# Kernel tuning notes

Hardware: AMD Instinct MI355X
Metric: run time of the kernel (lower is better)

## Reference

```python
import jax, jax.numpy as jnp
import numpy as np

B, L, D, H = 2, 2048, 1024, 16
Dh = D // H


def setup_inputs() -> dict:
    key = jax.random.key(0)
    k = jax.random.split(key, 6)
    s = 1.0 / np.sqrt(D).astype(np.float32)
    return {
        "x": jax.random.normal(k[0], (B, L, D), jnp.float32),
        "mask": jnp.ones((B, L), jnp.int32),
        "user_emb": jax.random.normal(k[1], (B, D), jnp.float32),
        "W_q": jax.random.normal(k[2], (D, D), jnp.float32) * s,
        "W_k": jax.random.normal(k[3], (D, D), jnp.float32) * s,
        "W_v": jax.random.normal(k[4], (D, D), jnp.float32) * s,
        "W_o": jax.random.normal(k[5], (D, D), jnp.float32) * s,
    }


def reference(x, mask, user_emb, W_q, W_k, W_v, W_o):
    b, l, d = x.shape
    # torch nn.Linear(bias=False): y = x @ W.T
    Q = x @ W_q.T
    K = x @ W_k.T
    V = x @ W_v.T

    def split(t):  # [B,L,D] -> [B,H,L,Dh]
        return t.reshape(b, l, H, Dh).transpose(0, 2, 1, 3)

    Qh, Kh, Vh = split(Q), split(K), split(V)

    # additive_bias: rank-1 per-head user bias, [B,H,L,1]
    u = user_emb.reshape(b, H, Dh)
    bias = jnp.einsum('bhld,bhd->bhl', Qh, u)[..., None]

    scores = jnp.einsum('bhld,bhmd->bhlm', Qh, Kh) / np.float32(np.sqrt(Dh))
    scores = scores + bias
    # padding mask: 1 = valid, 0 = pad (broadcast over query dim)
    scores = jnp.where(mask[:, None, None, :] == 0, -jnp.inf, scores)
    # causal mask
    causal = jnp.triu(jnp.ones((l, l), jnp.bool_), k=1)
    scores = jnp.where(causal, -jnp.inf, scores)

    attn = jax.nn.softmax(scores, axis=-1)  # dropout p=0 -> identity
    ctx = jnp.einsum('bhlm,bhmd->bhld', attn, Vh)
    out = ctx.transpose(0, 2, 1, 3).reshape(b, l, d)
    return out @ W_o.T
```

## Files before the change

### kernel.cpp

```cpp
#include <hip/hip_runtime.h>
#include <hip/hip_bf16.h>
#include <stdint.h>

#define Bc 2
#define Lc 2048
#define Dc 1024
#define Hc 16
#define DHc 64

using f32x4  = __attribute__((ext_vector_type(4))) float;
using f32x16 = __attribute__((ext_vector_type(16))) float;
using bf16x8 = __attribute__((ext_vector_type(8))) short;
using bf16x4 = __attribute__((ext_vector_type(4))) short;

static __device__ __forceinline__ unsigned short f2bf(float f) {
  __hip_bfloat16 h = __float2bfloat16(f);
  return __builtin_bit_cast(unsigned short, h);
}
static __device__ __forceinline__ float bf2f(unsigned short u) {
  unsigned int x = ((unsigned int)u) << 16;
  return __builtin_bit_cast(float, x);
}
static __device__ __forceinline__ unsigned int pk2(float a, float b) {
  return (unsigned int)f2bf(a) | ((unsigned int)f2bf(b) << 16);
}

static __device__ __forceinline__ void gload16(const void* g, void* l) {
  __builtin_amdgcn_global_load_lds(
      (const __attribute__((address_space(1))) unsigned int*)g,
      (__attribute__((address_space(3))) unsigned int*)l, 16, 0, 0);
}

__global__ __launch_bounds__(256) void cvt_kernel(
    const float* __restrict__ x,  const float* __restrict__ wq,
    const float* __restrict__ wk, const float* __restrict__ wv,
    const float* __restrict__ wo,
    unsigned short* __restrict__ xb,  unsigned short* __restrict__ wqb,
    unsigned short* __restrict__ wkb, unsigned short* __restrict__ wvb,
    unsigned short* __restrict__ wob) {
  int i = (blockIdx.x * 256 + threadIdx.x) * 4;
  const float* src; unsigned short* dst; int off;
  if (i < 4194304) { src = x; dst = xb; off = i; }
  else {
    int j = i - 4194304; int w = j >> 20; off = j & 1048575;
    src = w == 0 ? wq : w == 1 ? wk : w == 2 ? wv : wo;
    dst = w == 0 ? wqb : w == 1 ? wkb : w == 2 ? wvb : wob;
  }
  float4 v = *(const float4*)(src + off);
  ushort4 u;
  u.x = f2bf(v.x); u.y = f2bf(v.y); u.z = f2bf(v.z); u.w = f2bf(v.w);
  *(ushort4*)(dst + off) = u;
}

template <int MODE>
static __device__ __forceinline__ void gemm_body(
    const unsigned short* __restrict__ A, const unsigned short* __restrict__ Bw,
    void* __restrict__ Cout, float scale, char* As, char* Bs, int tm, int tn) {
  const int t = threadIdx.x, w = t >> 6, l = t & 63;
  const int wr = w >> 1, wc = w & 1;
  const int K = 1024;
  f32x4 zz = {0.f, 0.f, 0.f, 0.f};
  f32x4 acc[4][4];
  for (int a = 0; a < 4; a++)
    for (int b = 0; b < 4; b++) acc[a][b] = zz;
  const char* Ag = (const char*)A;
  const char* Bg = (const char*)Bw;
  for (int k0 = 0; k0 < K; k0 += 32) {
#pragma unroll
    for (int i = 0; i < 2; i++) {
      int s = i * 256 + w * 64 + l;
      gload16(Ag + ((tm + (s >> 2)) * K + k0 + (s & 3) * 8) * 2,
              As + (i * 256 + w * 64) * 16);
      gload16(Bg + ((tn + (s >> 2)) * K + k0 + (s & 3) * 8) * 2,
              Bs + (i * 256 + w * 64) * 16);
    }
    __syncthreads();
    bf16x8 af[4], bfg[4];
#pragma unroll
    for (int mm = 0; mm < 4; mm++)
      af[mm] = *(const bf16x8*)(As + (wr * 64 + mm * 16 + (l & 15)) * 64 + (l >> 4) * 16);
#pragma unroll
    for (int nn = 0; nn < 4; nn++)
      bfg[nn] = *(const bf16x8*)(Bs + (wc * 64 + nn * 16 + (l & 15)) * 64 + (l >> 4) * 16);
#pragma unroll
    for (int mm = 0; mm < 4; mm++)
#pragma unroll
      for (int nn = 0; nn < 4; nn++)
        acc[mm][nn] = __builtin_amdgcn_mfma_f32_16x16x32_bf16(af[mm], bfg[nn], acc[mm][nn], 0, 0, 0);
    __syncthreads();
  }
#pragma unroll
  for (int mm = 0; mm < 4; mm++) {
#pragma unroll
    for (int nn = 0; nn < 4; nn++) {
      int col = tn + wc * 64 + nn * 16 + (l & 15);
#pragma unroll
      for (int r = 0; r < 4; r++) {
        int row = tm + wr * 64 + mm * 16 + (l >> 4) * 4 + r;
        if (MODE == 0) {
          int b = row >> 11, ll = row & 2047, h = col >> 6, d = col & 63;
          ((unsigned short*)Cout)[(((b * Hc + h) << 11) + ll) * 64 + d] =
              f2bf(acc[mm][nn][r] * scale);
        } else if (MODE == 1) {
          ((float*)Cout)[row * 1024 + col] = acc[mm][nn][r];
        } else {
          int h = row >> 6, d = row & 63, b = col >> 11, ll = col & 2047;
          ((unsigned short*)Cout)[(((b * Hc + h) * 64 + d) << 11) + ll] =
              f2bf(acc[mm][nn][r]);
        }
      }
    }
  }
}

__global__ __launch_bounds__(256) void gemm_qkv(
    const unsigned short* __restrict__ xb,
    const unsigned short* __restrict__ wq, const unsigned short* __restrict__ wk,
    const unsigned short* __restrict__ wv,
    unsigned short* __restrict__ q, unsigned short* __restrict__ k,
    unsigned short* __restrict__ vT) {
  __shared__ char lds[16384];
  int z = blockIdx.z;
  if (z < 2) {
    gemm_body<0>(xb, z == 0 ? wq : wk, z == 0 ? q : k,
                 z == 0 ? 0.125f * 1.44269504089f : 1.0f,
                 lds, lds + 8192, blockIdx.x * 128, blockIdx.y * 128);
  } else {
    gemm_body<2>(wv, xb, vT, 1.0f, lds, lds + 8192,
                 blockIdx.y * 128, blockIdx.x * 128);
  }
}

__global__ __launch_bounds__(256) void gemm_out(
    const unsigned short* __restrict__ ctx, const unsigned short* __restrict__ wo,
    float* __restrict__ out) {
  __shared__ char lds[16384];
  gemm_body<1>(ctx, wo, out, 1.0f, lds, lds + 8192,
               blockIdx.x * 128, blockIdx.y * 128);
}

__global__ __launch_bounds__(256, 4) void attn_kernel(
    const unsigned short* __restrict__ Q, const unsigned short* __restrict__ Kg,
    const unsigned short* __restrict__ VT,
    unsigned short* __restrict__ Op, float2* __restrict__ ml) {
  __shared__ char lds[32768];
  const int t = threadIdx.x, w = t >> 6, l = t & 63;
  const int hi = l >> 5, q32 = l & 31;
  const int idx = blockIdx.x;
  const int bh = idx & 31;
  const int g = idx >> 5;
  const int qt = 15 - (g >> 1);
  const int c = g & 1;
  const int h1 = qt + 1;
  const int kb0 = c ? h1 : 0;
  const int kb1 = c ? 2 * h1 : h1;
  const unsigned short* Qb = Q + bh * (Lc * DHc);
  const unsigned short* Kb = Kg + bh * (Lc * DHc);
  const unsigned short* Vb = VT + bh * (Lc * DHc);
  const int qrow = qt * 128 + w * 32 + q32;

  bf16x8 qf[4];
#pragma unroll
  for (int s = 0; s < 4; s++)
    qf[s] = *(const bf16x8*)(Qb + qrow * 64 + s * 16 + hi * 8);

  const f32x16 z16 = {0.f,0.f,0.f,0.f,0.f,0.f,0.f,0.f,
                      0.f,0.f,0.f,0.f,0.f,0.f,0.f,0.f};
  float mi = -1e30f, li = 0.f;
  f32x16 accO[2];
  accO[0] = z16; accO[1] = z16;

  const int s0i = w * 64 + l;
  auto stage = [&](int bi, int kb) {
    char* Ksb = lds + bi * 8192;
    char* Vsb = lds + 16384 + bi * 8192;
#pragma unroll
    for (int i = 0; i < 2; i++) {
      int s = i * 256 + s0i;
      int row = s >> 3;
      int cb = ((s & 7) * 16) ^ ((row & 7) << 4);
      gload16((const char*)Kb + (kb * 64 + row) * 128 + cb,
              Ksb + (i * 256 + w * 64) * 16);
      gload16((const char*)Vb + row * 4096 + kb * 128 + cb,
              Vsb + (i * 256 + w * 64) * 16);
    }
  };

  stage(0, kb0);
  __syncthreads();
  for (int kb = kb0; kb < kb1; ++kb) {
    const int cur = (kb - kb0) & 1;
    char* Ks = lds + cur * 8192;
    char* Vs = lds + 16384 + cur * 8192;
    if (kb + 1 < kb1) stage(cur ^ 1, kb + 1);

    f32x16 sf[2];
    sf[0] = z16; sf[1] = z16;
    __builtin_amdgcn_s_setprio(1);
#pragma unroll
    for (int blk = 0; blk < 2; blk++) {
      int row = blk * 32 + q32;
      int rsw = (row & 7) << 4;
#pragma unroll
      for (int s = 0; s < 4; s++) {
        bf16x8 kf = *(const bf16x8*)(Ks + row * 128 + (((2 * s + hi) * 16) ^ rsw));
        sf[blk] = __builtin_amdgcn_mfma_f32_32x32x16_bf16(kf, qf[s], sf[blk], 0, 0, 0);
      }
    }
    __builtin_amdgcn_s_setprio(0);

    if (kb * 64 + 63 > qt * 128 + w * 32) {
#pragma unroll
      for (int blk = 0; blk < 2; blk++)
#pragma unroll
        for (int r = 0; r < 16; r++) {
          int kg = kb * 64 + blk * 32 + (r & 3) + 8 * (r >> 2) + 4 * hi;
          if (kg > qrow) sf[blk][r] = -1e30f;
        }
    }

    float tm16[16];
#pragma unroll
    for (int r = 0; r < 16; r++) tm16[r] = fmaxf(sf[0][r], sf[1][r]);
#pragma unroll
    for (int r = 0; r < 8; r++) tm16[r] = fmaxf(tm16[r], tm16[r + 8]);
#pragma unroll
    for (int r = 0; r < 4; r++) tm16[r] = fmaxf(tm16[r], tm16[r + 4]);
    float pm = fmaxf(fmaxf(tm16[0], tm16[1]), fmaxf(tm16[2], tm16[3]));
    pm = fmaxf(pm, __shfl_xor(pm, 32));

    if (!__all(pm - mi <= 8.f)) {
      float corr = __builtin_amdgcn_exp2f(mi - pm);
      mi = pm;
      li *= corr;
#pragma unroll
      for (int db = 0; db < 2; db++)
#pragma unroll
        for (int r = 0; r < 16; r++) accO[db][r] *= corr;
    }

    float a16[16];
#pragma unroll
    for (int r = 0; r < 16; r++) {
      float p0 = __builtin_amdgcn_exp2f(sf[0][r] - mi);
      float p1 = __builtin_amdgcn_exp2f(sf[1][r] - mi);
      sf[0][r] = p0; sf[1][r] = p1;
      a16[r] = p0 + p1;
    }
#pragma unroll
    for (int r = 0; r < 8; r++) a16[r] += a16[r + 8];
#pragma unroll
    for (int r = 0; r < 4; r++) a16[r] += a16[r + 4];
    float rs = (a16[0] + a16[1]) + (a16[2] + a16[3]);
    rs += __shfl_xor(rs, 32);
    li += rs;

    bf16x8 pf[4];
#pragma unroll
    for (int kw = 0; kw < 4; kw++) {
      const int bkl = kw >> 1, o = (kw & 1) * 8;
      unsigned int a01 = pk2(sf[bkl][o + 0], sf[bkl][o + 1]);
      unsigned int a23 = pk2(sf[bkl][o + 2], sf[bkl][o + 3]);
      unsigned int b01 = pk2(sf[bkl][o + 4], sf[bkl][o + 5]);
      unsigned int b23 = pk2(sf[bkl][o + 6], sf[bkl][o + 7]);
      auto s1 = __builtin_amdgcn_permlane32_swap(a01, b01, false, false);
      auto s2 = __builtin_amdgcn_permlane32_swap(a23, b23, false, false);
      uint4 uu;
      uu.x = s1[0];
      uu.y = s2[0];
      uu.z = s1[1];
      uu.w = s2[1];
      pf[kw] = __builtin_bit_cast(bf16x8, uu);
    }

    __builtin_amdgcn_s_setprio(1);
#pragma unroll
    for (int kw = 0; kw < 4; kw++) {
#pragma unroll
      for (int db = 0; db < 2; db++) {
        int row = db * 32 + q32;
        int rsw = (row & 7) << 4;
        bf16x8 vf = *(const bf16x8*)(Vs + row * 128 + (((2 * kw + hi) * 16) ^ rsw));
        accO[db] = __builtin_amdgcn_mfma_f32_32x32x16_bf16(vf, pf[kw], accO[db], 0, 0, 0);
      }
    }
    __builtin_amdgcn_s_setprio(0);
    __syncthreads();
  }

  unsigned short* Opc = Op + idx * 8192;
  const int ql = w * 32 + q32;
#pragma unroll
  for (int db = 0; db < 2; db++)
#pragma unroll
    for (int rq = 0; rq < 4; rq++) {
      int d0 = db * 32 + 8 * rq + 4 * hi;
      bf16x4 v4;
#pragma unroll
      for (int j = 0; j < 4; j++) v4[j] = (short)f2bf(accO[db][rq * 4 + j]);
      *(bf16x4*)(Opc + ql * 64 + d0) = v4;
    }
  if (hi == 0) ml[idx * 128 + ql] = make_float2(mi, li);
}

__global__ __launch_bounds__(256) void combine_kernel(
    const unsigned short* __restrict__ Op, const float2* __restrict__ ml,
    unsigned short* __restrict__ ctx) {
  const int cb = blockIdx.x;
  const int bh = cb & 31, qt = cb >> 5;
  const int i0 = ((15 - qt) * 2) * 32 + bh;
  const int i1 = i0 + 32;
  const int t = threadIdx.x;
  const int ql = t >> 1, dh = (t & 1) * 32;
  float2 p0 = ml[i0 * 128 + ql];
  float2 p1 = ml[i1 * 128 + ql];
  float m = fmaxf(p0.x, p1.x);
  float e0 = __builtin_amdgcn_exp2f(p0.x - m);
  float e1 = __builtin_amdgcn_exp2f(p1.x - m);
  float inv = 1.0f / (p0.y * e0 + p1.y * e1);
  float s0 = e0 * inv, s1 = e1 * inv;
  const int b = bh >> 4, h = bh & 15;
  unsigned short* dst = ctx + (size_t)(b * Lc + qt * 128 + ql) * Dc + h * 64 + dh;
  const unsigned short* q0 = Op + i0 * 8192 + ql * 64 + dh;
  const unsigned short* q1 = Op + i1 * 8192 + ql * 64 + dh;
#pragma unroll
  for (int seg = 0; seg < 4; seg++) {
    bf16x8 o0 = *(const bf16x8*)(q0 + seg * 8);
    bf16x8 o1 = *(const bf16x8*)(q1 + seg * 8);
    bf16x8 outv;
#pragma unroll
    for (int j = 0; j < 8; j++)
      outv[j] = (short)f2bf(bf2f((unsigned short)o0[j]) * s0 +
                            bf2f((unsigned short)o1[j]) * s1);
    *(bf16x8*)(dst + seg * 8) = outv;
  }
}

extern "C" void kernel_launch(void* const* d_in, const int* in_sizes, int n_in,
                              void* d_out, int out_size, void* d_ws, size_t ws_size,
                              hipStream_t stream) {
  const float* x  = (const float*)d_in[0];
  const float* Wq = (const float*)d_in[3];
  const float* Wk = (const float*)d_in[4];
  const float* Wv = (const float*)d_in[5];
  const float* Wo = (const float*)d_in[6];

  char* ws = (char*)d_ws;
  const size_t MB = 1024 * 1024;
  unsigned short* xb  = (unsigned short*)(ws);
  unsigned short* wqb = (unsigned short*)(ws + 8 * MB);
  unsigned short* wkb = (unsigned short*)(ws + 10 * MB);
  unsigned short* wvb = (unsigned short*)(ws + 12 * MB);
  unsigned short* q   = (unsigned short*)(ws + 16 * MB);
  unsigned short* k   = (unsigned short*)(ws + 24 * MB);
  unsigned short* vT  = (unsigned short*)(ws + 32 * MB);
  unsigned short* ctx = (unsigned short*)(ws + 40 * MB);
  unsigned short* wob = (unsigned short*)(ws + 48 * MB);
  unsigned short* Op  = (unsigned short*)(ws);
  float2*         ml  = (float2*)(ws + 50 * MB);

  cvt_kernel<<<8192, 256, 0, stream>>>(x, Wq, Wk, Wv, Wo, xb, wqb, wkb, wvb, wob);
  gemm_qkv<<<dim3(32, 8, 3), 256, 0, stream>>>(xb, wqb, wkb, wvb, q, k, vT);
  attn_kernel<<<1024, 256, 0, stream>>>(q, k, vT, Op, ml);
  combine_kernel<<<512, 256, 0, stream>>>(Op, ml, ctx);
  gemm_out<<<dim3(32, 8, 1), 256, 0, stream>>>(ctx, wob, (float*)d_out);
}
```

Measured before the change: 110.1 us.

## Rebalance causal attention split-K work via lookup table and write unsplit tiles directly

Replaces the uniform two-way split of each query tile's key range with a 36-entry table of (query tile, key range) chunks. Short tiles run unsplit and write normalized context directly, while long tiles are split into 2-4 chunks that the combine kernel merges, for 1152 roughly equal-sized blocks. It also swaps one __syncthreads per iteration for explicit vmcnt waits plus s_barrier so the prefetch of the next tile can stay in flight, and uses v_cvt_pk_bf16_f32 for packing. The aim is to cut tail imbalance and combine traffic, at the cost of table lookups and a combine over a variable number of chunks.

```diff
diff --git a/kernel.cpp b/kernel.cpp
--- a/kernel.cpp
+++ b/kernel.cpp
@@ -21,8 +21,10 @@
   unsigned int x = ((unsigned int)u) << 16;
   return __builtin_bit_cast(float, x);
 }
-static __device__ __forceinline__ unsigned int pk2(float a, float b) {
-  return (unsigned int)f2bf(a) | ((unsigned int)f2bf(b) << 16);
+static __device__ __forceinline__ unsigned int cvtpk(float a, float b) {
+  unsigned int r;
+  asm("v_cvt_pk_bf16_f32 %0, %1, %2" : "=v"(r) : "v"(a), "v"(b));
+  return r;
 }
 
 static __device__ __forceinline__ void gload16(const void* g, void* l) {
@@ -139,21 +141,26 @@
                blockIdx.x * 128, blockIdx.y * 128);
 }
 
+__device__ const int g_qt[36]  = {7,6,5,15,15,15,15,14,14,11,11,11,10,4,13,13,13,13,14,14,12,12,10,10,9,9,3,12,12,9,8,8,8,2,1,0};
+__device__ const int g_kb0[36] = {0,0,0,0,8,16,24,0,8,0,8,16,0,0,0,7,14,21,16,23,0,7,8,15,0,7,0,14,20,14,0,6,12,0,0,0};
+__device__ const int g_kb1[36] = {16,14,12,8,16,24,32,8,16,8,16,24,8,10,7,14,21,28,23,30,7,14,15,22,7,14,8,20,26,20,6,12,18,6,4,2};
+__device__ const int g_pid[36] = {-1,-1,-1,0,1,2,3,4,5,16,17,18,19,-1,8,9,10,11,6,7,12,13,20,21,22,23,-1,14,15,24,25,26,27,-1,-1,-1};
+
 __global__ __launch_bounds__(256, 4) void attn_kernel(
     const unsigned short* __restrict__ Q, const unsigned short* __restrict__ Kg,
     const unsigned short* __restrict__ VT,
-    unsigned short* __restrict__ Op, float2* __restrict__ ml) {
+    unsigned short* __restrict__ Op, float2* __restrict__ ml,
+    unsigned short* __restrict__ ctx) {
   __shared__ char lds[32768];
   const int t = threadIdx.x, w = t >> 6, l = t & 63;
   const int hi = l >> 5, q32 = l & 31;
   const int idx = blockIdx.x;
   const int bh = idx & 31;
   const int g = idx >> 5;
-  const int qt = 15 - (g >> 1);
-  const int c = g & 1;
-  const int h1 = qt + 1;
-  const int kb0 = c ? h1 : 0;
-  const int kb1 = c ? 2 * h1 : h1;
+  const int qt  = g_qt[g];
+  const int kb0 = g_kb0[g];
+  const int kb1 = g_kb1[g];
+  const int pid = g_pid[g];
   const unsigned short* Qb = Q + bh * (Lc * DHc);
   const unsigned short* Kb = Kg + bh * (Lc * DHc);
   const unsigned short* Vb = VT + bh * (Lc * DHc);
@@ -187,12 +194,19 @@
   };
 
   stage(0, kb0);
-  __syncthreads();
   for (int kb = kb0; kb < kb1; ++kb) {
     const int cur = (kb - kb0) & 1;
     char* Ks = lds + cur * 8192;
     char* Vs = lds + 16384 + cur * 8192;
-    if (kb + 1 < kb1) stage(cur ^ 1, kb + 1);
+    if (kb + 1 < kb1) {
+      stage(cur ^ 1, kb + 1);
+      asm volatile("s_waitcnt vmcnt(4)" ::: "memory");
+    } else {
+      asm volatile("s_waitcnt vmcnt(0)" ::: "memory");
+    }
+    __builtin_amdgcn_sched_barrier(0);
+    __builtin_amdgcn_s_barrier();
+    __builtin_amdgcn_sched_barrier(0);
 
     f32x16 sf[2];
     sf[0] = z16; sf[1] = z16;
@@ -259,10 +273,10 @@
 #pragma unroll
     for (int kw = 0; kw < 4; kw++) {
       const int bkl = kw >> 1, o = (kw & 1) * 8;
-      unsigned int a01 = pk2(sf[bkl][o + 0], sf[bkl][o + 1]);
-      unsigned int a23 = pk2(sf[bkl][o + 2], sf[bkl][o + 3]);
-      unsigned int b01 = pk2(sf[bkl][o + 4], sf[bkl][o + 5]);
-      unsigned int b23 = pk2(sf[bkl][o + 6], sf[bkl][o + 7]);
+      unsigned int a01 = cvtpk(sf[bkl][o + 0], sf[bkl][o + 1]);
+      unsigned int a23 = cvtpk(sf[bkl][o + 2], sf[bkl][o + 3]);
+      unsigned int b01 = cvtpk(sf[bkl][o + 4], sf[bkl][o + 5]);
+      unsigned int b23 = cvtpk(sf[bkl][o + 6], sf[bkl][o + 7]);
       auto s1 = __builtin_amdgcn_permlane32_swap(a01, b01, false, false);
       auto s2 = __builtin_amdgcn_permlane32_swap(a23, b23, false, false);
       uint4 uu;
@@ -285,53 +299,89 @@
       }
     }
     __builtin_amdgcn_s_setprio(0);
-    __syncthreads();
-  }
-
-  unsigned short* Opc = Op + idx * 8192;
-  const int ql = w * 32 + q32;
-#pragma unroll
-  for (int db = 0; db < 2; db++)
-#pragma unroll
-    for (int rq = 0; rq < 4; rq++) {
-      int d0 = db * 32 + 8 * rq + 4 * hi;
-      bf16x4 v4;
-#pragma unroll
-      for (int j = 0; j < 4; j++) v4[j] = (short)f2bf(accO[db][rq * 4 + j]);
-      *(bf16x4*)(Opc + ql * 64 + d0) = v4;
-    }
-  if (hi == 0) ml[idx * 128 + ql] = make_float2(mi, li);
-}
+    __builtin_amdgcn_sched_barrier(0);
+    __builtin_amdgcn_s_barrier();
+  }
+
+  const int b = bh >> 4, h = bh & 15;
+  if (pid < 0) {
+    float inv = 1.0f / li;
+    unsigned short* dst = ctx + (size_t)(b * Lc + qrow) * Dc + h * 64;
+#pragma unroll
+    for (int db = 0; db < 2; db++)
+#pragma unroll
+      for (int rq = 0; rq < 4; rq++) {
+        int d0 = db * 32 + 8 * rq + 4 * hi;
+        bf16x4 v4;
+#pragma unroll
+        for (int j = 0; j < 4; j++) v4[j] = (short)f2bf(accO[db][rq * 4 + j] * inv);
+        *(bf16x4*)(dst + d0) = v4;
+      }
+  } else {
+    unsigned short* Opc = Op + (size_t)(bh * 28 + pid) * 8192;
+    const int ql = w * 32 + q32;
+#pragma unroll
+    for (int db = 0; db < 2; db++)
+#pragma unroll
+      for (int rq = 0; rq < 4; rq++) {
+        int d0 = db * 32 + 8 * rq + 4 * hi;
+        bf16x4 v4;
+#pragma unroll
+        for (int j = 0; j < 4; j++) v4[j] = (short)f2bf(accO[db][rq * 4 + j]);
+        *(bf16x4*)(Opc + ql * 64 + d0) = v4;
+      }
+    if (hi == 0) ml[(bh * 28 + pid) * 128 + ql] = make_float2(mi, li);
+  }
+}
+
+__device__ const int c_pb[8]  = {25, 22, 19, 16, 12, 8, 4, 0};
+__device__ const int c_nch[8] = { 3,  3,  3,  3,  4, 4, 4, 4};
 
 __global__ __launch_bounds__(256) void combine_kernel(
     const unsigned short* __restrict__ Op, const float2* __restrict__ ml,
     unsigned short* __restrict__ ctx) {
   const int cb = blockIdx.x;
-  const int bh = cb & 31, qt = cb >> 5;
-  const int i0 = ((15 - qt) * 2) * 32 + bh;
-  const int i1 = i0 + 32;
+  const int qq = cb >> 5, bh = cb & 31;
+  const int qt = 8 + qq;
+  const int pb = c_pb[qq], nch = c_nch[qq];
   const int t = threadIdx.x;
   const int ql = t >> 1, dh = (t & 1) * 32;
-  float2 p0 = ml[i0 * 128 + ql];
-  float2 p1 = ml[i1 * 128 + ql];
-  float m = fmaxf(p0.x, p1.x);
-  float e0 = __builtin_amdgcn_exp2f(p0.x - m);
-  float e1 = __builtin_amdgcn_exp2f(p1.x - m);
-  float inv = 1.0f / (p0.y * e0 + p1.y * e1);
-  float s0 = e0 * inv, s1 = e1 * inv;
+  float2 pp[4];
+  float mx = -1e30f;
+#pragma unroll
+  for (int j = 0; j < 4; j++) {
+    int jj = j < nch ? j : 0;
+    float2 v = ml[(size_t)(bh * 28 + pb + jj) * 128 + ql];
+    pp[j] = (j < nch) ? v : make_float2(-1e30f, 0.f);
+    mx = fmaxf(mx, pp[j].x);
+  }
+  float wgt[4];
+  float den = 0.f;
+#pragma unroll
+  for (int j = 0; j < 4; j++) {
+    float e = __builtin_amdgcn_exp2f(pp[j].x - mx);
+    den += pp[j].y * e;
+    wgt[j] = e;
+  }
+  float inv = 1.0f / den;
+#pragma unroll
+  for (int j = 0; j < 4; j++) wgt[j] *= inv;
   const int b = bh >> 4, h = bh & 15;
   unsigned short* dst = ctx + (size_t)(b * Lc + qt * 128 + ql) * Dc + h * 64 + dh;
-  const unsigned short* q0 = Op + i0 * 8192 + ql * 64 + dh;
-  const unsigned short* q1 = Op + i1 * 8192 + ql * 64 + dh;
 #pragma unroll
   for (int seg = 0; seg < 4; seg++) {
-    bf16x8 o0 = *(const bf16x8*)(q0 + seg * 8);
-    bf16x8 o1 = *(const bf16x8*)(q1 + seg * 8);
+    float a8[8] = {0.f, 0.f, 0.f, 0.f, 0.f, 0.f, 0.f, 0.f};
+#pragma unroll
+    for (int j = 0; j < 4; j++) {
+      int jj = j < nch ? j : 0;
+      bf16x8 o = *(const bf16x8*)(Op + (size_t)(bh * 28 + pb + jj) * 8192 +
+                                  ql * 64 + dh + seg * 8);
+#pragma unroll
+      for (int e = 0; e < 8; e++) a8[e] += wgt[j] * bf2f((unsigned short)o[e]);
+    }
     bf16x8 outv;
 #pragma unroll
-    for (int j = 0; j < 8; j++)
-      outv[j] = (short)f2bf(bf2f((unsigned short)o0[j]) * s0 +
-                            bf2f((unsigned short)o1[j]) * s1);
+    for (int e = 0; e < 8; e++) outv[e] = (short)f2bf(a8[e]);
     *(bf16x8*)(dst + seg * 8) = outv;
   }
 }
@@ -361,7 +411,7 @@
 
   cvt_kernel<<<8192, 256, 0, stream>>>(x, Wq, Wk, Wv, Wo, xb, wqb, wkb, wvb, wob);
   gemm_qkv<<<dim3(32, 8, 3), 256, 0, stream>>>(xb, wqb, wkb, wvb, q, k, vT);
-  attn_kernel<<<1024, 256, 0, stream>>>(q, k, vT, Op, ml);
-  combine_kernel<<<512, 256, 0, stream>>>(Op, ml, ctx);
+  attn_kernel<<<1152, 256, 0, stream>>>(q, k, vT, Op, ml, ctx);
+  combine_kernel<<<256, 256, 0, stream>>>(Op, ml, ctx);
   gemm_out<<<dim3(32, 8, 1), 256, 0, stream>>>(ctx, wob, (float*)d_out);
 }
```

New measurement: 110.3 us. Within noise of the previous version (+0.2%).
